# Performance work log

Measured on AMD Instinct MI355X. Metric: run time of the kernel, lower is better.

## Reference

```python
import jax, jax.numpy as jnp
import numpy as np

B, L, D_MODEL = 8, 2048, 512
N_QUBITS, Q_LAYERS = 10, 4
DIM = 2 ** N_QUBITS
EPS = 1e-5  # torch LayerNorm default


def _apply_1q_tok(state, U, q):
    # per-token 2x2 gate U: (N,2,2), wire 0 = most significant (PennyLane order)
    N = state.shape[0]
    s = state.reshape(N, 2 ** q, 2, -1)
    return jnp.einsum('nij,najb->naib', U, s).reshape(N, -1)


def _apply_1q(state, U, q):
    # shared 2x2 gate U: (2,2)
    N = state.shape[0]
    s = state.reshape(N, 2 ** q, 2, -1)
    return jnp.einsum('ij,najb->naib', U, s).reshape(N, -1)


def _cnot(state, c, t):
    N = state.shape[0]
    lo, hi = min(c, t), max(c, t)
    s = state.reshape(N, 2 ** lo, 2, 2 ** (hi - lo - 1), 2, -1)
    if c < t:
        # control is the first 2-axis; flip target axis where control==1
        s = s.at[:, :, 1].set(jnp.flip(s[:, :, 1], axis=3))
    else:
        # target is the first 2-axis, control the second
        s = s.at[:, :, :, :, 1].set(jnp.flip(s[:, :, :, :, 1], axis=2))
    return s.reshape(N, -1)


def _simulate(feats, weights):
    # feats: (N, n_qubits) angles; weights: (q_layers, n_qubits, 2)
    N = feats.shape[0]
    half = 0.5 * feats
    cxa = jnp.cos(half).astype(jnp.complex64)
    sxa = jnp.sin(half).astype(jnp.complex64)
    phz = jnp.exp(1j * half.astype(jnp.complex64))  # e^{+i theta/2}
    state = jnp.zeros((N, DIM), jnp.complex64).at[:, 0].set(1.0 + 0j)
    for l in range(Q_LAYERS):
        # AngleEmbedding rotation='X' : RX(feat_q) on wire q
        for q in range(N_QUBITS):
            c, s = cxa[:, q], sxa[:, q]
            U = jnp.stack([jnp.stack([c, -1j * s], -1),
                           jnp.stack([-1j * s, c], -1)], -2)  # (N,2,2)
            state = _apply_1q_tok(state, U, q)
        # AngleEmbedding rotation='Z' : RZ(feat_q) on wire q (diagonal)
        for q in range(N_QUBITS):
            p = phz[:, q]
            diag = jnp.stack([jnp.conj(p), p], -1)  # (N,2)
            s = state.reshape(N, 2 ** q, 2, -1)
            state = (s * diag[:, None, :, None]).reshape(N, -1)
        # trainable RY, RZ per wire (shared across tokens)
        for q in range(N_QUBITS):
            ty = 0.5 * weights[l, q, 0]
            cy, sy = jnp.cos(ty), jnp.sin(ty)
            Uy = jnp.stack([jnp.stack([cy, -sy]), jnp.stack([sy, cy])]).astype(jnp.complex64)
            state = _apply_1q(state, Uy, q)
            pz = jnp.exp(1j * (0.5 * weights[l, q, 1]).astype(jnp.complex64))
            diag = jnp.stack([jnp.conj(pz), pz])  # (2,)
            s = state.reshape(N, 2 ** q, 2, -1)
            state = (s * diag[None, None, :, None]).reshape(N, -1)
        # entangling CNOT ring
        for q in range(N_QUBITS):
            state = _cnot(state, q, (q + 1) % N_QUBITS)
    probs = jnp.real(state) ** 2 + jnp.imag(state) ** 2  # (N, 2**n)
    zs = []
    for q in range(N_QUBITS):
        p = probs.reshape(N, 2 ** q, 2, -1).sum(axis=(1, 3))  # (N,2)
        zs.append(p[:, 0] - p[:, 1])  # <Z_q>
    return jnp.stack(zs, -1)  # (N, n_qubits)


def setup_inputs() -> dict:
    key = jax.random.key(0)
    ks = jax.random.split(key, 4)
    x = jax.random.normal(ks[0], (B, L, D_MODEL), jnp.float32)
    in_W = jax.random.normal(ks[1], (N_QUBITS, D_MODEL), jnp.float32) / np.float32(np.sqrt(D_MODEL))
    in_b = jnp.zeros((N_QUBITS,), jnp.float32)
    gamma = jnp.ones((N_QUBITS,), jnp.float32)
    beta = jnp.zeros((N_QUBITS,), jnp.float32)
    weights = 0.05 * jax.random.normal(ks[2], (Q_LAYERS, N_QUBITS, 2), jnp.float32)
    out_W = jax.random.normal(ks[3], (D_MODEL, N_QUBITS), jnp.float32) / np.float32(np.sqrt(N_QUBITS))
    out_b = jnp.zeros((D_MODEL,), jnp.float32)
    return {"x": x, "in_W": in_W, "in_b": in_b, "gamma": gamma, "beta": beta,
            "weights": weights, "out_W": out_W, "out_b": out_b}


def reference(x, in_W, in_b, gamma, beta, weights, out_W, out_b):
    Bs, Ls, _ = x.shape
    h = jnp.tanh(jnp.einsum('bld,qd->blq', x, in_W) + in_b)
    mu = h.mean(-1, keepdims=True)
    var = ((h - mu) ** 2).mean(-1, keepdims=True)
    h = (h - mu) / jnp.sqrt(var + EPS) * gamma + beta
    q_out = _simulate(h.reshape(Bs * Ls, N_QUBITS), weights)
    q_out = q_out.reshape(Bs, Ls, N_QUBITS).astype(x.dtype)
    return x + jnp.einsum('blq,dq->bld', q_out, out_W) + out_b
```

## Files before the change

kernel.cpp:

```cpp
#include <hip/hip_runtime.h>

#define NQ 10
#define DQ 512
#define QL 4
#define NTOK (8 * 2048)
#define QOFF (NQ * DQ)

typedef float v2f __attribute__((ext_vector_type(2)));
typedef float v4f __attribute__((ext_vector_type(4)));
typedef _Float16 h2 __attribute__((ext_vector_type(2)));

template <int CTRL>
__device__ __forceinline__ int dppi(int i) {
    return __builtin_amdgcn_update_dpp(i, i, CTRL, 0xF, 0xF, false);
}
template <int M>
__device__ __forceinline__ int lxi(int i) {
    if constexpr (M == 1)      return dppi<0xB1>(i);
    else if constexpr (M == 2) return dppi<0x4E>(i);
    else if constexpr (M == 8) return dppi<0x128>(i);
    else return __shfl_xor(i, M);
}
template <int M>
__device__ __forceinline__ float lx(float v) {
    return __builtin_bit_cast(float, lxi<M>(__builtin_bit_cast(int, v)));
}
template <int M>
__device__ __forceinline__ h2 lxh(h2 v) {
    return __builtin_bit_cast(h2, lxi<M>(__builtin_bit_cast(int, v)));
}

__device__ __forceinline__ void reduce10(float* z) {
#pragma unroll
    for (int q = 0; q < NQ; ++q) {
        z[q] += lx<32>(z[q]); z[q] += lx<16>(z[q]); z[q] += lx<8>(z[q]);
        z[q] += lx<4>(z[q]);  z[q] += lx<2>(z[q]);  z[q] += lx<1>(z[q]);
    }
}

__device__ __forceinline__ v4f coef(const v4f* Q, float c, float s) {
    float A = c * c, C = c * s;
    return Q[0] + A * Q[1] + C * Q[2];
}

__device__ __forceinline__ h2 h2bc(float v) {
    _Float16 h = (_Float16)v; return (h2){h, h};
}
__device__ __forceinline__ h2 h2swap(h2 v) {
    return __builtin_shufflevector(v, v, 1, 0);
}

template <int M>
__device__ __forceinline__ void gate_lane_h(h2* sr, h2* si, v4f cf, bool bit) {
    const float aif = bit ? -cf.y : cf.y;
    const float brf = bit ? cf.z : -cf.z;
    const h2 ar = h2bc(cf.x), ai = h2bc(aif), br = h2bc(brf), bi = h2bc(cf.w);
#pragma unroll
    for (int j = 0; j < 8; ++j) {
        h2 wr = lxh<M>(sr[j]), wi = lxh<M>(si[j]);
        h2 nr = ar * sr[j] - ai * si[j] + br * wr - bi * wi;
        h2 ni = ar * si[j] + ai * sr[j] + br * wi + bi * wr;
        sr[j] = nr; si[j] = ni;
    }
}
template <int BJ>
__device__ __forceinline__ void gate_reg_h(h2* sr, h2* si, v4f cf) {
    const h2 ar = h2bc(cf.x), ai = h2bc(cf.y), br = h2bc(cf.z), bi = h2bc(cf.w);
#pragma unroll
    for (int j = 0; j < 8; ++j) if (!(j & BJ)) {
        const int j1 = j | BJ;
        h2 x0r = sr[j], x0i = si[j], x1r = sr[j1], x1i = si[j1];
        sr[j]  = ar * x0r - ai * x0i - br * x1r - bi * x1i;
        si[j]  = ar * x0i + ai * x0r - br * x1i + bi * x1r;
        sr[j1] = br * x0r - bi * x0i + ar * x1r + ai * x1i;
        si[j1] = br * x0i + bi * x0r + ar * x1i - ai * x1r;
    }
}
__device__ __forceinline__ void gate_elem_h(h2* sr, h2* si, v4f cf) {
    const h2 ar = h2bc(cf.x), bi = h2bc(cf.w);
    const h2 aiV = (h2){(_Float16)cf.y, (_Float16)(-cf.y)};
    const h2 brV = (h2){(_Float16)(-cf.z), (_Float16)cf.z};
#pragma unroll
    for (int j = 0; j < 8; ++j) {
        h2 swr = h2swap(sr[j]), swi = h2swap(si[j]);
        h2 nr = ar * sr[j] - aiV * si[j] + brV * swr - bi * swi;
        h2 ni = ar * si[j] + aiV * sr[j] + brV * swi + bi * swr;
        sr[j] = nr; si[j] = ni;
    }
}

__device__ __forceinline__ void perm678_h(h2* a) {
    h2 o2 = a[2], o4 = a[4], o7 = a[7];
    a[1] = h2swap(a[1]);
    a[2] = a[3]; a[3] = h2swap(o2);
    a[4] = a[6]; a[6] = a[5]; a[5] = h2swap(o7); a[7] = h2swap(o4);
}

__device__ __forceinline__ void cnot_ring_h(h2* sr, h2* si, int lane, int srcl) {
#pragma unroll
    for (int j = 0; j < 8; ++j) {
        sr[j] = __builtin_bit_cast(h2, __shfl(__builtin_bit_cast(int, sr[j]), srcl));
        si[j] = __builtin_bit_cast(h2, __shfl(__builtin_bit_cast(int, si[j]), srcl));
    }
    {
        const bool ctrl = (lane & 1);
#pragma unroll
        for (int j = 0; j < 4; ++j) {
            h2 t0 = sr[j], t1 = sr[j + 4];
            sr[j] = ctrl ? t1 : t0; sr[j + 4] = ctrl ? t0 : t1;
            t0 = si[j]; t1 = si[j + 4];
            si[j] = ctrl ? t1 : t0; si[j + 4] = ctrl ? t0 : t1;
        }
    }
    perm678_h(sr);
    perm678_h(si);
#pragma unroll
    for (int j = 0; j < 8; ++j) {
        h2 w = lxh<32>(sr[j]); sr[j] = (h2){sr[j].x, w.y};
        w = lxh<32>(si[j]);    si[j] = (h2){si[j].x, w.y};
    }
}

__global__ __launch_bounds__(512) void prep_kernel(
    const float* __restrict__ weights, const float* __restrict__ out_W,
    float* __restrict__ ws)
{
    const int t = threadIdx.x;
#pragma unroll
    for (int q = 0; q < NQ; ++q)
        ws[q * DQ + t] = out_W[t * NQ + q];
    if (t < QL * NQ) {
        float w0 = weights[t * 2], w1 = weights[t * 2 + 1];
        float cy = __cosf(0.5f * w0), sy = __sinf(0.5f * w0);
        float cz = __cosf(0.5f * w1), sz = __sinf(0.5f * w1);
        float d = cy - sy, e = cy + sy;
        v4f* Q = (v4f*)(ws + QOFF);
        Q[t * 3 + 0] = (v4f){-cz * sy,  sz * sy,  cz * cy,  sz * cy};
        Q[t * 3 + 1] = (v4f){ cz * e,  -sz * e,  -cz * d,  -sz * d};
        Q[t * 3 + 2] = (v4f){-sz * d,  -cz * d,   sz * e,  -cz * e};
    }
}

__global__ __launch_bounds__(256) void quantum_kernel(
    const float* __restrict__ x, const float* __restrict__ in_W,
    const float* __restrict__ in_b, const float* __restrict__ gamma,
    const float* __restrict__ beta, const float* __restrict__ ws,
    const float* __restrict__ out_b, float* __restrict__ out)
{
    const int t = threadIdx.x;
    const int lane = t & 63;
    const int tok = blockIdx.x * 4 + (t >> 6);
    const v4f* Qg = (const v4f*)(ws + QOFF);

    int srcl = lane;
#pragma unroll
    for (int q = 4; q >= 0; --q) {
        const int bc = 5 - q, bt = bc - 1;
        srcl ^= ((srcl >> bc) & 1) << bt;
    }

    const v2f* xrow2 = (const v2f*)(x + (size_t)tok * DQ);
    const v2f* inW2 = (const v2f*)in_W;
    v2f hv[NQ];
#pragma unroll
    for (int q = 0; q < NQ; ++q) hv[q] = (v2f){0.f, 0.f};
#pragma unroll
    for (int k = 0; k < 4; ++k) {
        v2f xk = xrow2[lane + 64 * k];
#pragma unroll
        for (int q = 0; q < NQ; ++q)
            hv[q] = xk * inW2[q * (DQ / 2) + lane + 64 * k] + hv[q];
    }
    float h[NQ];
#pragma unroll
    for (int q = 0; q < NQ; ++q) h[q] = hv[q].x + hv[q].y;
    reduce10(h);

    float mu = 0.f;
#pragma unroll
    for (int q = 0; q < NQ; ++q) {
        float e = __expf(2.f * (h[q] + in_b[q]));
        h[q] = (e - 1.f) * __builtin_amdgcn_rcpf(e + 1.f);
        mu += h[q];
    }
    mu *= 0.1f;
    float var = 0.f;
#pragma unroll
    for (int q = 0; q < NQ; ++q) { float d0 = h[q] - mu; var += d0 * d0; }
    var *= 0.1f;
    const float rstd = rsqrtf(var + 1e-5f);

    float cq[NQ], sq[NQ];
#pragma unroll
    for (int q = 0; q < NQ; ++q) {
        float f = (h[q] - mu) * rstd * gamma[q] + beta[q];
        float hf = 0.5f * f;
        cq[q] = __cosf(hf);
        sq[q] = __sinf(hf);
    }

    h2 sr[8], si[8];
    {
        const v4f* Q0 = Qg;
        v4f f0 = coef(Q0 + 0, cq[0], sq[0]);
        bool b0 = (lane & 32);
        float Lr = b0 ? f0.z : f0.x, Li = b0 ? f0.w : f0.y;
#pragma unroll
        for (int q = 1; q < 6; ++q) {
            v4f f = coef(Q0 + 3 * q, cq[q], sq[q]);
            bool b = lane & (1 << (5 - q));
            float fr = b ? f.z : f.x, fi = b ? f.w : f.y;
            float nr = Lr * fr - Li * fi, ni = Lr * fi + Li * fr;
            Lr = nr; Li = ni;
        }
        float Pr[8], Pi[8];
        {
            v4f f6 = coef(Q0 + 18, cq[6], sq[6]);
            Pr[0] = Lr * f6.x - Li * f6.y; Pi[0] = Lr * f6.y + Li * f6.x;
            Pr[4] = Lr * f6.z - Li * f6.w; Pi[4] = Lr * f6.w + Li * f6.z;
        }
        {
            v4f f7 = coef(Q0 + 21, cq[7], sq[7]);
#pragma unroll
            for (int jj = 0; jj < 8; jj += 4) {
                float tr1 = Pr[jj] * f7.z - Pi[jj] * f7.w;
                float ti1 = Pr[jj] * f7.w + Pi[jj] * f7.z;
                float tr0 = Pr[jj] * f7.x - Pi[jj] * f7.y;
                float ti0 = Pr[jj] * f7.y + Pi[jj] * f7.x;
                Pr[jj] = tr0; Pi[jj] = ti0; Pr[jj + 2] = tr1; Pi[jj + 2] = ti1;
            }
        }
        {
            v4f f8 = coef(Q0 + 24, cq[8], sq[8]);
#pragma unroll
            for (int jj = 0; jj < 8; jj += 2) {
                float tr1 = Pr[jj] * f8.z - Pi[jj] * f8.w;
                float ti1 = Pr[jj] * f8.w + Pi[jj] * f8.z;
                float tr0 = Pr[jj] * f8.x - Pi[jj] * f8.y;
                float ti0 = Pr[jj] * f8.y + Pi[jj] * f8.x;
                Pr[jj] = tr0; Pi[jj] = ti0; Pr[jj + 1] = tr1; Pi[jj + 1] = ti1;
            }
        }
        {
            v4f f9 = coef(Q0 + 27, cq[9], sq[9]);
#pragma unroll
            for (int j = 0; j < 8; ++j) {
                float e0r = Pr[j] * f9.x - Pi[j] * f9.y;
                float e0i = Pr[j] * f9.y + Pi[j] * f9.x;
                float e1r = Pr[j] * f9.z - Pi[j] * f9.w;
                float e1i = Pr[j] * f9.w + Pi[j] * f9.z;
                sr[j] = (h2){(_Float16)e0r, (_Float16)e1r};
                si[j] = (h2){(_Float16)e0i, (_Float16)e1i};
            }
        }
    }
    cnot_ring_h(sr, si, lane, srcl);

#pragma unroll
    for (int l = 1; l < QL; ++l) {
        const v4f* Ql = Qg + l * NQ * 3;
        gate_lane_h<32>(sr, si, coef(Ql + 0,  cq[0], sq[0]), lane & 32);
        gate_lane_h< 8>(sr, si, coef(Ql + 6,  cq[2], sq[2]), lane & 8);
        gate_lane_h<16>(sr, si, coef(Ql + 3,  cq[1], sq[1]), lane & 16);
        gate_lane_h< 2>(sr, si, coef(Ql + 12, cq[4], sq[4]), lane & 2);
        gate_lane_h< 4>(sr, si, coef(Ql + 9,  cq[3], sq[3]), lane & 4);
        gate_lane_h< 1>(sr, si, coef(Ql + 15, cq[5], sq[5]), lane & 1);
        gate_reg_h<4>(sr, si, coef(Ql + 18, cq[6], sq[6]));
        gate_reg_h<2>(sr, si, coef(Ql + 21, cq[7], sq[7]));
        gate_reg_h<1>(sr, si, coef(Ql + 24, cq[8], sq[8]));
        gate_elem_h(sr, si, coef(Ql + 27, cq[9], sq[9]));
        cnot_ring_h(sr, si, lane, srcl);
    }

    v2f aP = {0.f, 0.f}, a6 = {0.f, 0.f}, a7 = {0.f, 0.f}, a8 = {0.f, 0.f};
#pragma unroll
    for (int j = 0; j < 8; ++j) {
        v2f rr = {(float)sr[j].x, (float)sr[j].y};
        v2f ii = {(float)si[j].x, (float)si[j].y};
        v2f p = rr * rr + ii * ii;
        aP += p;
        if (j & 4) a6 -= p; else a6 += p;
        if (j & 2) a7 -= p; else a7 += p;
        if (j & 1) a8 -= p; else a8 += p;
    }
    const float P = aP.x + aP.y;
    float z[NQ];
#pragma unroll
    for (int q = 0; q < 6; ++q)
        z[q] = (lane & (1 << (5 - q))) ? -P : P;
    z[6] = a6.x + a6.y; z[7] = a7.x + a7.y; z[8] = a8.x + a8.y;
    z[9] = aP.x - aP.y;
    reduce10(z);

    v2f* orow2 = (v2f*)(out + (size_t)tok * DQ);
    const v2f* ob2 = (const v2f*)out_b;
    const v2f* oWt2 = (const v2f*)ws;
#pragma unroll
    for (int k = 0; k < 4; ++k) {
        const int d2 = lane + 64 * k;
        v2f acc = xrow2[d2] + ob2[d2];
#pragma unroll
        for (int q = 0; q < NQ; ++q)
            acc = z[q] * oWt2[q * (DQ / 2) + d2] + acc;
        orow2[d2] = acc;
    }
}

extern "C" void kernel_launch(void* const* d_in, const int* in_sizes, int n_in,
                              void* d_out, int out_size, void* d_ws, size_t ws_size,
                              hipStream_t stream) {
    const float* x       = (const float*)d_in[0];
    const float* in_W    = (const float*)d_in[1];
    const float* in_b    = (const float*)d_in[2];
    const float* gamma   = (const float*)d_in[3];
    const float* beta    = (const float*)d_in[4];
    const float* weights = (const float*)d_in[5];
    const float* out_W   = (const float*)d_in[6];
    const float* out_b   = (const float*)d_in[7];
    float* out = (float*)d_out;
    float* ws = (float*)d_ws;

    hipLaunchKernelGGL(prep_kernel, dim3(1), dim3(512), 0, stream,
                       weights, out_W, ws);
    hipLaunchKernelGGL(quantum_kernel, dim3(NTOK / 4), dim3(256), 0, stream,
                       x, in_W, in_b, gamma, beta, ws, out_b, out);
}
```

Baseline: 198.8 us.

## Fold final CNOT ring into measurement parity and use bpermute for cross-lane swaps

The last CNOT ring is dropped: its permutation is folded into the Z-expectation signs, which are now computed from lane-bit parities and register-index XOR parities. Cross-lane exchanges for xor 32/16/4 go through ds_bpermute with precomputed addresses instead of generic shuffles, and the ring's permutation shuffle uses a precomputed bpermute address. Gate coefficients take precomputed c*c and c*s, and fp16 packing uses the cvt_pkrtz intrinsic. The aim is fewer cross-lane operations and less conversion work, at the cost of more intricate sign bookkeeping and round-toward-zero packing.

```diff
diff --git a/kernel.cpp b/kernel.cpp
--- a/kernel.cpp
+++ b/kernel.cpp
@@ -10,54 +10,83 @@
 typedef float v4f __attribute__((ext_vector_type(4)));
 typedef _Float16 h2 __attribute__((ext_vector_type(2)));
 
+__device__ __forceinline__ int bperm(int addr, int v) {
+    return __builtin_amdgcn_ds_bpermute(addr, v);
+}
+__device__ __forceinline__ float bpermf(int addr, float v) {
+    return __builtin_bit_cast(float, bperm(addr, __builtin_bit_cast(int, v)));
+}
+__device__ __forceinline__ h2 bpermh(int addr, h2 v) {
+    return __builtin_bit_cast(h2, bperm(addr, __builtin_bit_cast(int, v)));
+}
 template <int CTRL>
 __device__ __forceinline__ int dppi(int i) {
     return __builtin_amdgcn_update_dpp(i, i, CTRL, 0xF, 0xF, false);
 }
 template <int M>
-__device__ __forceinline__ int lxi(int i) {
-    if constexpr (M == 1)      return dppi<0xB1>(i);
-    else if constexpr (M == 2) return dppi<0x4E>(i);
-    else if constexpr (M == 8) return dppi<0x128>(i);
-    else return __shfl_xor(i, M);
+__device__ __forceinline__ float dppxf(float v) {
+    int i = __builtin_bit_cast(int, v);
+    if constexpr (M == 1)      i = dppi<0xB1>(i);
+    else if constexpr (M == 2) i = dppi<0x4E>(i);
+    else                       i = dppi<0x128>(i);
+    return __builtin_bit_cast(float, i);
 }
 template <int M>
-__device__ __forceinline__ float lx(float v) {
-    return __builtin_bit_cast(float, lxi<M>(__builtin_bit_cast(int, v)));
-}
-template <int M>
-__device__ __forceinline__ h2 lxh(h2 v) {
-    return __builtin_bit_cast(h2, lxi<M>(__builtin_bit_cast(int, v)));
-}
-
-__device__ __forceinline__ void reduce10(float* z) {
+__device__ __forceinline__ h2 dppxh(h2 v) {
+    return __builtin_bit_cast(h2, __builtin_bit_cast(float, v) * 0.f + 0.f), v;
+}
+
+__device__ __forceinline__ void reduce10(float* z, int a32, int a16, int a4) {
 #pragma unroll
     for (int q = 0; q < NQ; ++q) {
-        z[q] += lx<32>(z[q]); z[q] += lx<16>(z[q]); z[q] += lx<8>(z[q]);
-        z[q] += lx<4>(z[q]);  z[q] += lx<2>(z[q]);  z[q] += lx<1>(z[q]);
-    }
-}
-
-__device__ __forceinline__ v4f coef(const v4f* Q, float c, float s) {
-    float A = c * c, C = c * s;
+        z[q] += bpermf(a32, z[q]);
+        z[q] += bpermf(a16, z[q]);
+        z[q] += dppxf<8>(z[q]);
+        z[q] += bpermf(a4, z[q]);
+        z[q] += dppxf<2>(z[q]);
+        z[q] += dppxf<1>(z[q]);
+    }
+}
+
+__device__ __forceinline__ v4f coef(const v4f* Q, float A, float C) {
     return Q[0] + A * Q[1] + C * Q[2];
 }
-
-__device__ __forceinline__ h2 h2bc(float v) {
-    _Float16 h = (_Float16)v; return (h2){h, h};
-}
+__device__ __forceinline__ h2 pk2(float a, float b) {
+    return __builtin_bit_cast(h2, __builtin_amdgcn_cvt_pkrtz(a, b));
+}
+__device__ __forceinline__ h2 h2bc(float v) { return pk2(v, v); }
 __device__ __forceinline__ h2 h2swap(h2 v) {
     return __builtin_shufflevector(v, v, 1, 0);
 }
 
-template <int M>
-__device__ __forceinline__ void gate_lane_h(h2* sr, h2* si, v4f cf, bool bit) {
+__device__ __forceinline__ void gate_lane_hp(h2* sr, h2* si, v4f cf, bool bit, int addr) {
     const float aif = bit ? -cf.y : cf.y;
     const float brf = bit ? cf.z : -cf.z;
     const h2 ar = h2bc(cf.x), ai = h2bc(aif), br = h2bc(brf), bi = h2bc(cf.w);
 #pragma unroll
     for (int j = 0; j < 8; ++j) {
-        h2 wr = lxh<M>(sr[j]), wi = lxh<M>(si[j]);
+        h2 wr = bpermh(addr, sr[j]), wi = bpermh(addr, si[j]);
+        h2 nr = ar * sr[j] - ai * si[j] + br * wr - bi * wi;
+        h2 ni = ar * si[j] + ai * sr[j] + br * wi + bi * wr;
+        sr[j] = nr; si[j] = ni;
+    }
+}
+template <int M>
+__device__ __forceinline__ void gate_lane_hd(h2* sr, h2* si, v4f cf, bool bit) {
+    const float aif = bit ? -cf.y : cf.y;
+    const float brf = bit ? cf.z : -cf.z;
+    const h2 ar = h2bc(cf.x), ai = h2bc(aif), br = h2bc(brf), bi = h2bc(cf.w);
+#pragma unroll
+    for (int j = 0; j < 8; ++j) {
+        h2 wr, wi;
+        {
+            int iR = __builtin_bit_cast(int, sr[j]);
+            int iI = __builtin_bit_cast(int, si[j]);
+            if constexpr (M == 1)      { iR = dppi<0xB1>(iR);  iI = dppi<0xB1>(iI); }
+            else if constexpr (M == 2) { iR = dppi<0x4E>(iR);  iI = dppi<0x4E>(iI); }
+            else                       { iR = dppi<0x128>(iR); iI = dppi<0x128>(iI); }
+            wr = __builtin_bit_cast(h2, iR); wi = __builtin_bit_cast(h2, iI);
+        }
         h2 nr = ar * sr[j] - ai * si[j] + br * wr - bi * wi;
         h2 ni = ar * si[j] + ai * sr[j] + br * wi + bi * wr;
         sr[j] = nr; si[j] = ni;
@@ -78,8 +107,8 @@
 }
 __device__ __forceinline__ void gate_elem_h(h2* sr, h2* si, v4f cf) {
     const h2 ar = h2bc(cf.x), bi = h2bc(cf.w);
-    const h2 aiV = (h2){(_Float16)cf.y, (_Float16)(-cf.y)};
-    const h2 brV = (h2){(_Float16)(-cf.z), (_Float16)cf.z};
+    const h2 aiV = pk2(cf.y, -cf.y);
+    const h2 brV = pk2(-cf.z, cf.z);
 #pragma unroll
     for (int j = 0; j < 8; ++j) {
         h2 swr = h2swap(sr[j]), swi = h2swap(si[j]);
@@ -96,11 +125,11 @@
     a[4] = a[6]; a[6] = a[5]; a[5] = h2swap(o7); a[7] = h2swap(o4);
 }
 
-__device__ __forceinline__ void cnot_ring_h(h2* sr, h2* si, int lane, int srcl) {
-#pragma unroll
-    for (int j = 0; j < 8; ++j) {
-        sr[j] = __builtin_bit_cast(h2, __shfl(__builtin_bit_cast(int, sr[j]), srcl));
-        si[j] = __builtin_bit_cast(h2, __shfl(__builtin_bit_cast(int, si[j]), srcl));
+__device__ __forceinline__ void cnot_ring_h(h2* sr, h2* si, int lane, int apm, int a32) {
+#pragma unroll
+    for (int j = 0; j < 8; ++j) {
+        sr[j] = bpermh(apm, sr[j]);
+        si[j] = bpermh(apm, si[j]);
     }
     {
         const bool ctrl = (lane & 1);
@@ -116,8 +145,8 @@
     perm678_h(si);
 #pragma unroll
     for (int j = 0; j < 8; ++j) {
-        h2 w = lxh<32>(sr[j]); sr[j] = (h2){sr[j].x, w.y};
-        w = lxh<32>(si[j]);    si[j] = (h2){si[j].x, w.y};
+        h2 w = bpermh(a32, sr[j]); sr[j] = (h2){sr[j].x, w.y};
+        w = bpermh(a32, si[j]);    si[j] = (h2){si[j].x, w.y};
     }
 }
 
@@ -152,12 +181,16 @@
     const int tok = blockIdx.x * 4 + (t >> 6);
     const v4f* Qg = (const v4f*)(ws + QOFF);
 
+    const int a32 = (lane ^ 32) << 2;
+    const int a16 = (lane ^ 16) << 2;
+    const int a4  = (lane ^ 4)  << 2;
     int srcl = lane;
 #pragma unroll
     for (int q = 4; q >= 0; --q) {
         const int bc = 5 - q, bt = bc - 1;
         srcl ^= ((srcl >> bc) & 1) << bt;
     }
+    const int apm = srcl << 2;
 
     const v2f* xrow2 = (const v2f*)(x + (size_t)tok * DQ);
     const v2f* inW2 = (const v2f*)in_W;
@@ -174,7 +207,7 @@
     float h[NQ];
 #pragma unroll
     for (int q = 0; q < NQ; ++q) h[q] = hv[q].x + hv[q].y;
-    reduce10(h);
+    reduce10(h, a32, a16, a4);
 
     float mu = 0.f;
 #pragma unroll
@@ -190,24 +223,25 @@
     var *= 0.1f;
     const float rstd = rsqrtf(var + 1e-5f);
 
-    float cq[NQ], sq[NQ];
+    float Aq[NQ], Cq[NQ];
 #pragma unroll
     for (int q = 0; q < NQ; ++q) {
         float f = (h[q] - mu) * rstd * gamma[q] + beta[q];
         float hf = 0.5f * f;
-        cq[q] = __cosf(hf);
-        sq[q] = __sinf(hf);
+        float c = __cosf(hf), s = __sinf(hf);
+        Aq[q] = c * c;
+        Cq[q] = c * s;
     }
 
     h2 sr[8], si[8];
     {
         const v4f* Q0 = Qg;
-        v4f f0 = coef(Q0 + 0, cq[0], sq[0]);
+        v4f f0 = coef(Q0 + 0, Aq[0], Cq[0]);
         bool b0 = (lane & 32);
         float Lr = b0 ? f0.z : f0.x, Li = b0 ? f0.w : f0.y;
 #pragma unroll
         for (int q = 1; q < 6; ++q) {
-            v4f f = coef(Q0 + 3 * q, cq[q], sq[q]);
+            v4f f = coef(Q0 + 3 * q, Aq[q], Cq[q]);
             bool b = lane & (1 << (5 - q));
             float fr = b ? f.z : f.x, fi = b ? f.w : f.y;
             float nr = Lr * fr - Li * fi, ni = Lr * fi + Li * fr;
@@ -215,12 +249,12 @@
         }
         float Pr[8], Pi[8];
         {
-            v4f f6 = coef(Q0 + 18, cq[6], sq[6]);
+            v4f f6 = coef(Q0 + 18, Aq[6], Cq[6]);
             Pr[0] = Lr * f6.x - Li * f6.y; Pi[0] = Lr * f6.y + Li * f6.x;
             Pr[4] = Lr * f6.z - Li * f6.w; Pi[4] = Lr * f6.w + Li * f6.z;
         }
         {
-            v4f f7 = coef(Q0 + 21, cq[7], sq[7]);
+            v4f f7 = coef(Q0 + 21, Aq[7], Cq[7]);
 #pragma unroll
             for (int jj = 0; jj < 8; jj += 4) {
                 float tr1 = Pr[jj] * f7.z - Pi[jj] * f7.w;
@@ -231,7 +265,7 @@
             }
         }
         {
-            v4f f8 = coef(Q0 + 24, cq[8], sq[8]);
+            v4f f8 = coef(Q0 + 24, Aq[8], Cq[8]);
 #pragma unroll
             for (int jj = 0; jj < 8; jj += 2) {
                 float tr1 = Pr[jj] * f8.z - Pi[jj] * f8.w;
@@ -242,55 +276,70 @@
             }
         }
         {
-            v4f f9 = coef(Q0 + 27, cq[9], sq[9]);
+            v4f f9 = coef(Q0 + 27, Aq[9], Cq[9]);
 #pragma unroll
             for (int j = 0; j < 8; ++j) {
                 float e0r = Pr[j] * f9.x - Pi[j] * f9.y;
                 float e0i = Pr[j] * f9.y + Pi[j] * f9.x;
                 float e1r = Pr[j] * f9.z - Pi[j] * f9.w;
                 float e1i = Pr[j] * f9.w + Pi[j] * f9.z;
-                sr[j] = (h2){(_Float16)e0r, (_Float16)e1r};
-                si[j] = (h2){(_Float16)e0i, (_Float16)e1i};
+                sr[j] = pk2(e0r, e1r);
+                si[j] = pk2(e0i, e1i);
             }
         }
     }
-    cnot_ring_h(sr, si, lane, srcl);
+    cnot_ring_h(sr, si, lane, apm, a32);
 
 #pragma unroll
     for (int l = 1; l < QL; ++l) {
         const v4f* Ql = Qg + l * NQ * 3;
-        gate_lane_h<32>(sr, si, coef(Ql + 0,  cq[0], sq[0]), lane & 32);
-        gate_lane_h< 8>(sr, si, coef(Ql + 6,  cq[2], sq[2]), lane & 8);
-        gate_lane_h<16>(sr, si, coef(Ql + 3,  cq[1], sq[1]), lane & 16);
-        gate_lane_h< 2>(sr, si, coef(Ql + 12, cq[4], sq[4]), lane & 2);
-        gate_lane_h< 4>(sr, si, coef(Ql + 9,  cq[3], sq[3]), lane & 4);
-        gate_lane_h< 1>(sr, si, coef(Ql + 15, cq[5], sq[5]), lane & 1);
-        gate_reg_h<4>(sr, si, coef(Ql + 18, cq[6], sq[6]));
-        gate_reg_h<2>(sr, si, coef(Ql + 21, cq[7], sq[7]));
-        gate_reg_h<1>(sr, si, coef(Ql + 24, cq[8], sq[8]));
-        gate_elem_h(sr, si, coef(Ql + 27, cq[9], sq[9]));
-        cnot_ring_h(sr, si, lane, srcl);
-    }
-
-    v2f aP = {0.f, 0.f}, a6 = {0.f, 0.f}, a7 = {0.f, 0.f}, a8 = {0.f, 0.f};
+        gate_lane_hp(sr, si, coef(Ql + 0,  Aq[0], Cq[0]), lane & 32, a32);
+        gate_lane_hd<8>(sr, si, coef(Ql + 6,  Aq[2], Cq[2]), lane & 8);
+        gate_lane_hp(sr, si, coef(Ql + 3,  Aq[1], Cq[1]), lane & 16, a16);
+        gate_lane_hd<2>(sr, si, coef(Ql + 12, Aq[4], Cq[4]), lane & 2);
+        gate_lane_hp(sr, si, coef(Ql + 9,  Aq[3], Cq[3]), lane & 4, a4);
+        gate_lane_hd<1>(sr, si, coef(Ql + 15, Aq[5], Cq[5]), lane & 1);
+        gate_reg_h<4>(sr, si, coef(Ql + 18, Aq[6], Cq[6]));
+        gate_reg_h<2>(sr, si, coef(Ql + 21, Aq[7], Cq[7]));
+        gate_reg_h<1>(sr, si, coef(Ql + 24, Aq[8], Cq[8]));
+        gate_elem_h(sr, si, coef(Ql + 27, Aq[9], Cq[9]));
+        if (l < QL - 1) cnot_ring_h(sr, si, lane, apm, a32);
+    }
+
+    v2f aP = {0.f, 0.f}, a6 = {0.f, 0.f}, a7 = {0.f, 0.f}, aT = {0.f, 0.f};
 #pragma unroll
     for (int j = 0; j < 8; ++j) {
         v2f rr = {(float)sr[j].x, (float)sr[j].y};
         v2f ii = {(float)si[j].x, (float)si[j].y};
         v2f p = rr * rr + ii * ii;
         aP += p;
-        if (j & 4) a6 -= p; else a6 += p;
-        if (j & 2) a7 -= p; else a7 += p;
-        if (j & 1) a8 -= p; else a8 += p;
-    }
-    const float P = aP.x + aP.y;
+        a6 += (j & 4) ? -p : p;
+        a7 += ((((j >> 2) ^ (j >> 1)) & 1)) ? -p : p;
+        aT += ((((j >> 2) ^ (j >> 1) ^ j) & 1)) ? -p : p;
+    }
+    const float A0 = aP.x + aP.y;
+    const float B6 = a6.x + a6.y;
+    const float B7 = a7.x + a7.y;
+    const float B8 = aT.x + aT.y;
+    const float B9 = aT.x - aT.y;
+    const bool P1 = __popc(lane & 0x30) & 1;
+    const bool P2 = __popc(lane & 0x38) & 1;
+    const bool P3 = __popc(lane & 0x3C) & 1;
+    const bool P4 = __popc(lane & 0x3E) & 1;
+    const bool P5 = __popc(lane & 0x3F) & 1;
+    const bool PX = __popc(lane & 0x1F) & 1;
     float z[NQ];
-#pragma unroll
-    for (int q = 0; q < 6; ++q)
-        z[q] = (lane & (1 << (5 - q))) ? -P : P;
-    z[6] = a6.x + a6.y; z[7] = a7.x + a7.y; z[8] = a8.x + a8.y;
-    z[9] = aP.x - aP.y;
-    reduce10(z);
+    z[0] = PX ? -B9 : B9;
+    z[1] = P1 ? -A0 : A0;
+    z[2] = P2 ? -A0 : A0;
+    z[3] = P3 ? -A0 : A0;
+    z[4] = P4 ? -A0 : A0;
+    z[5] = P5 ? -A0 : A0;
+    z[6] = P5 ? -B6 : B6;
+    z[7] = P5 ? -B7 : B7;
+    z[8] = P5 ? -B8 : B8;
+    z[9] = P5 ? -B9 : B9;
+    reduce10(z, a32, a16, a4);
 
     v2f* orow2 = (v2f*)(out + (size_t)tok * DQ);
     const v2f* ob2 = (const v2f*)out_b;
```

Result: no change. 195.5 us (-1.7%).
